# Performance work log

Measured on AMD Instinct MI355X. Metric: run time of the kernel, lower is better.

Reference implementation:

```python
import jax, jax.numpy as jnp
import numpy as np

NUM_HEADS = 4


def setup_inputs() -> dict:
    key = jax.random.key(0)
    ks = jax.random.split(key, 9)
    B, C, H, W = 8, 128, 48, 48
    s = 0.02
    return {
        "x": jax.random.normal(ks[0], (B, C, H, W), dtype=jnp.float32),
        "Wq": jax.random.normal(ks[1], (C, C), dtype=jnp.float32) * s,
        "bq": jax.random.normal(ks[2], (C,), dtype=jnp.float32) * s,
        "Wk": jax.random.normal(ks[3], (C, C), dtype=jnp.float32) * s,
        "bk": jax.random.normal(ks[4], (C,), dtype=jnp.float32) * s,
        "Wv": jax.random.normal(ks[5], (C, C), dtype=jnp.float32) * s,
        "bv": jax.random.normal(ks[6], (C,), dtype=jnp.float32) * s,
        "Wo": jax.random.normal(ks[7], (C, C), dtype=jnp.float32) * s,
        "bo": jax.random.normal(ks[8], (C,), dtype=jnp.float32) * s,
    }


def reference(x, Wq, bq, Wk, bk, Wv, bv, Wo, bo):
    B, C, H, W = x.shape
    nh = NUM_HEADS
    hd = C // nh  # head_size
    S = H * W
    # b c h w -> b (h w) c
    xf = x.reshape(B, C, S).transpose(0, 2, 1)
    # nn.Linear: y = x @ W.T + b ; split heads: b s (h d) -> b h s d
    q = (xf @ Wq.T + bq).reshape(B, S, nh, hd).transpose(0, 2, 1, 3)
    k = (xf @ Wk.T + bk).reshape(B, S, nh, hd).transpose(0, 2, 1, 3)
    v = (xf @ Wv.T + bv).reshape(B, S, nh, hd).transpose(0, 2, 1, 3)
    # scores: [B, nh, S, S]
    scores = jnp.einsum('bhqd,bhkd->bhqk', q, k) / jnp.sqrt(jnp.float32(hd)).astype(x.dtype)
    attn = jax.nn.softmax(scores, axis=-1)
    ctx = jnp.einsum('bhqk,bhkd->bhqd', attn, v)
    # merge heads: b h s d -> b s (h d)
    ctx = ctx.transpose(0, 2, 1, 3).reshape(B, S, C)
    out = ctx @ Wo.T + bo  # [B, S, C]
    # b (h w) c -> b c h w
    return out.transpose(0, 2, 1).reshape(B, C, H, W)
```

## Files before the change

kernel.cpp:

```cpp
#include <hip/hip_runtime.h>
#include <hip/hip_bf16.h>

typedef __attribute__((ext_vector_type(8))) short bf16x8;
typedef __attribute__((ext_vector_type(4))) float floatx4;

constexpr int NB  = 8;
constexpr int NC  = 128;
constexpr int NS  = 2304;
constexpr int NNH = 4;
constexpr float SCALE_LOG2E = 0.17677669529663687f * 1.4426950408889634f;

__device__ inline unsigned short f2bf(float f) {
    union { float f; unsigned u; } v; v.f = f;
    unsigned r = v.u + 0x7FFF + ((v.u >> 16) & 1);
    return (unsigned short)(r >> 16);
}

__device__ inline float fexp2(float x) {
#if __has_builtin(__builtin_amdgcn_exp2f)
    return __builtin_amdgcn_exp2f(x);
#else
    return exp2f(x);
#endif
}

__device__ inline __hip_bfloat162 pk(float a, float b) {
    return __float22bfloat162_rn(make_float2(a, b));
}

__global__ __launch_bounds__(256) void qkv_fused_kernel(
    const float* __restrict__ x,
    const float* __restrict__ Wq, const float* __restrict__ bq,
    const float* __restrict__ Wk, const float* __restrict__ bk,
    const float* __restrict__ Wv, const float* __restrict__ bv,
    unsigned short* __restrict__ Qb, unsigned short* __restrict__ Kb,
    unsigned short* __restrict__ Vb)
{
    const int s0 = blockIdx.x * 64;
    const int b  = blockIdx.y;
    const int t  = threadIdx.x;
    const int w = t >> 6, lane = t & 63;
    const int l15 = lane & 15, quad = lane >> 4;

    __shared__ __align__(16) char smem[34304];
    float* tileF = (float*)(smem + w * 4224);
    unsigned short* xs = (unsigned short*)(smem + 16896);

    #pragma unroll
    for (int sh = 0; sh < 2; ++sh) {
        #pragma unroll
        for (int it = 0; it < 16; ++it) {
            int c = it * 2 + (lane >> 5), sl = lane & 31;
            tileF[c * 33 + sl] =
                x[((size_t)b * NC + 32 * w + c) * NS + s0 + 32 * sh + sl];
        }
        #pragma unroll
        for (int it = 0; it < 16; ++it) {
            int s_l = it * 2 + (lane >> 5), c_l = lane & 31;
            xs[(32 * sh + s_l) * 136 + 32 * w + c_l] =
                f2bf(tileF[c_l * 33 + s_l]);
        }
    }
    __syncthreads();

    bf16x8 a[4][4];
    #pragma unroll
    for (int m = 0; m < 4; ++m)
        #pragma unroll
        for (int c = 0; c < 4; ++c)
            a[m][c] = *(const bf16x8*)&xs[(16 * m + l15) * 136 + 32 * c + 8 * quad];
    __syncthreads();

    const int h = w;
    const size_t bh = (size_t)(b * NNH + h);
    unsigned short* e = (unsigned short*)smem + (size_t)w * 2560;

    for (int p = 0; p < 3; ++p) {
        const float* Wsel = (p == 0) ? Wq : (p == 1) ? Wk : Wv;
        const float* bsel = (p == 0) ? bq : (p == 1) ? bk : bv;
        const float sc = (p == 0) ? SCALE_LOG2E : 1.0f;

        bf16x8 wf[2][4];
        #pragma unroll
        for (int n = 0; n < 2; ++n)
            #pragma unroll
            for (int c = 0; c < 4; ++c) {
                const float* wp = &Wsel[(size_t)(32 * w + 16 * n + l15) * NC + 32 * c + 8 * quad];
                float4 wa = *(const float4*)wp;
                float4 wb = *(const float4*)(wp + 4);
                union { bf16x8 v; __hip_bfloat162 h2[4]; } u;
                u.h2[0] = pk(wa.x, wa.y);
                u.h2[1] = pk(wa.z, wa.w);
                u.h2[2] = pk(wb.x, wb.y);
                u.h2[3] = pk(wb.z, wb.w);
                wf[n][c] = u.v;
            }

        floatx4 acc[4][2] = {};
        #pragma unroll
        for (int c = 0; c < 4; ++c)
            #pragma unroll
            for (int m = 0; m < 4; ++m)
                #pragma unroll
                for (int n = 0; n < 2; ++n)
                    acc[m][n] = __builtin_amdgcn_mfma_f32_16x16x32_bf16(
                        a[m][c], wf[n][c], acc[m][n], 0, 0, 0);

        const float bj0 = bsel[32 * w + l15];
        const float bj1 = bsel[32 * w + 16 + l15];

        #pragma unroll
        for (int m = 0; m < 4; ++m)
            #pragma unroll
            for (int r = 0; r < 4; ++r) {
                e[(16 * m + 4 * quad + r) * 40 + l15]      = f2bf((acc[m][0][r] + bj0) * sc);
                e[(16 * m + 4 * quad + r) * 40 + 16 + l15] = f2bf((acc[m][1][r] + bj1) * sc);
            }

        if (p < 2) {
            unsigned short* dst = (p == 0) ? Qb : Kb;
            const int s_l = lane >> 1, half = lane & 1;
            #pragma unroll
            for (int sh = 0; sh < 2; ++sh) {
                bf16x8 v0 = *(const bf16x8*)&e[(sh * 32 + s_l) * 40 + 16 * half];
                bf16x8 v1 = *(const bf16x8*)&e[(sh * 32 + s_l) * 40 + 16 * half + 8];
                unsigned short* g = &dst[(bh * NS + s0 + sh * 32 + s_l) * 32 + 16 * half];
                *(bf16x8*)g = v0;
                *(bf16x8*)(g + 8) = v1;
            }
        } else {
            const int d = lane >> 1, half = lane & 1;
            #pragma unroll
            for (int sh = 0; sh < 2; ++sh) {
                unsigned short tmp[16];
                #pragma unroll
                for (int i = 0; i < 16; ++i) {
                    int pos = 16 * half + i;
                    int kl = (((pos >> 2) & 1) << 4) | (((pos >> 3) & 3) << 2) | (pos & 3);
                    tmp[i] = e[(sh * 32 + kl) * 40 + d];
                }
                unsigned short* g = &Vb[(bh * 32 + d) * NS + s0 + sh * 32 + 16 * half];
                *(bf16x8*)g = *(bf16x8*)&tmp[0];
                *(bf16x8*)(g + 8) = *(bf16x8*)&tmp[8];
            }
        }
    }
}

__global__ __launch_bounds__(512) void attn_out_kernel(
    const unsigned short* __restrict__ Qb,
    const unsigned short* __restrict__ Kb,
    const unsigned short* __restrict__ Vb,
    const float* __restrict__ Wo, const float* __restrict__ bo,
    float* __restrict__ out)
{
    const int bid = blockIdx.x;
    const int qt = bid >> 3, b = bid & 7;
    const int t = threadIdx.x;
    const int w = t >> 6, lane = t & 63;
    const int l15 = lane & 15, quad = lane >> 4;
    const int h = w & 3, ks = w >> 2;

    const size_t bh = (size_t)(b * NNH + h);
    const unsigned short* Kp = Kb + bh * NS * 32;
    const unsigned short* Vp = Vb + bh * 32 * NS;
    const int q0g = qt * 64;

    __shared__ __align__(16) float Osum[4][64 * 36];
    __shared__ float Ls[4][64];
    __shared__ __align__(16) unsigned short ctxs[64 * 136];

    bf16x8 qf[4];
    #pragma unroll
    for (int g = 0; g < 4; ++g)
        qf[g] = *(const bf16x8*)&Qb[(bh * NS + q0g + g * 16 + l15) * 32 + quad * 8];

    float lsum[4] = {};
    floatx4 o[4][2] = {};

    const int kbase = ks * 18 * 64;
    bf16x8 kfc[4], vfc[4], kfn[4], vfn[4];
    #pragma unroll
    for (int n = 0; n < 4; ++n)
        kfc[n] = *(const bf16x8*)&Kp[(kbase + 16 * n + l15) * 32 + quad * 8];
    vfc[0] = *(const bf16x8*)&Vp[(0  + l15) * NS + kbase +  0 + 8 * quad];
    vfc[1] = *(const bf16x8*)&Vp[(0  + l15) * NS + kbase + 32 + 8 * quad];
    vfc[2] = *(const bf16x8*)&Vp[(16 + l15) * NS + kbase +  0 + 8 * quad];
    vfc[3] = *(const bf16x8*)&Vp[(16 + l15) * NS + kbase + 32 + 8 * quad];

    for (int it = 0; it < 18; ++it) {
        const int kn = kbase + ((it < 17) ? (it + 1) * 64 : 0);
        #pragma unroll
        for (int n = 0; n < 4; ++n)
            kfn[n] = *(const bf16x8*)&Kp[(kn + 16 * n + l15) * 32 + quad * 8];
        vfn[0] = *(const bf16x8*)&Vp[(0  + l15) * NS + kn +  0 + 8 * quad];
        vfn[1] = *(const bf16x8*)&Vp[(0  + l15) * NS + kn + 32 + 8 * quad];
        vfn[2] = *(const bf16x8*)&Vp[(16 + l15) * NS + kn +  0 + 8 * quad];
        vfn[3] = *(const bf16x8*)&Vp[(16 + l15) * NS + kn + 32 + 8 * quad];

        #pragma unroll
        for (int g = 0; g < 4; ++g) {
            floatx4 s[4];
            #pragma unroll
            for (int n = 0; n < 4; ++n) {
                floatx4 z = {0.f, 0.f, 0.f, 0.f};
                s[n] = __builtin_amdgcn_mfma_f32_16x16x32_bf16(kfc[n], qf[g], z, 0, 0, 0);
            }
            float p[4][4];
            #pragma unroll
            for (int n = 0; n < 4; ++n)
                #pragma unroll
                for (int r = 0; r < 4; ++r) {
                    p[n][r] = fexp2(s[n][r]);
                    lsum[g] += p[n][r];
                }
            union { bf16x8 v; __hip_bfloat162 h2[4]; } pf0, pf1;
            pf0.h2[0] = pk(p[0][0], p[0][1]);
            pf0.h2[1] = pk(p[0][2], p[0][3]);
            pf0.h2[2] = pk(p[1][0], p[1][1]);
            pf0.h2[3] = pk(p[1][2], p[1][3]);
            pf1.h2[0] = pk(p[2][0], p[2][1]);
            pf1.h2[1] = pk(p[2][2], p[2][3]);
            pf1.h2[2] = pk(p[3][0], p[3][1]);
            pf1.h2[3] = pk(p[3][2], p[3][3]);

            o[g][0] = __builtin_amdgcn_mfma_f32_16x16x32_bf16(vfc[0], pf0.v, o[g][0], 0, 0, 0);
            o[g][0] = __builtin_amdgcn_mfma_f32_16x16x32_bf16(vfc[1], pf1.v, o[g][0], 0, 0, 0);
            o[g][1] = __builtin_amdgcn_mfma_f32_16x16x32_bf16(vfc[2], pf0.v, o[g][1], 0, 0, 0);
            o[g][1] = __builtin_amdgcn_mfma_f32_16x16x32_bf16(vfc[3], pf1.v, o[g][1], 0, 0, 0);
        }

        #pragma unroll
        for (int n = 0; n < 4; ++n) { kfc[n] = kfn[n]; vfc[n] = vfn[n]; }
    }

    #pragma unroll
    for (int g = 0; g < 4; ++g) {
        lsum[g] += __shfl_xor(lsum[g], 16);
        lsum[g] += __shfl_xor(lsum[g], 32);
    }

    if (ks == 0) {
        #pragma unroll
        for (int g = 0; g < 4; ++g)
            #pragma unroll
            for (int m = 0; m < 2; ++m)
                *(floatx4*)&Osum[h][(g * 16 + l15) * 36 + m * 16 + 4 * quad] = o[g][m];
        if (quad == 0)
            #pragma unroll
            for (int g = 0; g < 4; ++g)
                Ls[h][g * 16 + l15] = lsum[g];
    }
    __syncthreads();
    if (ks == 1) {
        #pragma unroll
        for (int g = 0; g < 4; ++g) {
            const float inv = 1.f / (Ls[h][g * 16 + l15] + lsum[g]);
            #pragma unroll
            for (int m = 0; m < 2; ++m) {
                floatx4 part = *(const floatx4*)&Osum[h][(g * 16 + l15) * 36 + m * 16 + 4 * quad];
                floatx4 tot = part + o[g][m];
                unsigned short* cx = &ctxs[(g * 16 + l15) * 136 + h * 32 + m * 16 + 4 * quad];
                *(__hip_bfloat162*)&cx[0] = pk(tot[0] * inv, tot[1] * inv);
                *(__hip_bfloat162*)&cx[2] = pk(tot[2] * inv, tot[3] * inv);
            }
        }
    }
    __syncthreads();

    const int j0 = w * 16;
    bf16x8 wo[4];
    #pragma unroll
    for (int c = 0; c < 4; ++c) {
        const float* wp = &Wo[(size_t)(j0 + l15) * NC + 32 * c + 8 * quad];
        float4 wa = *(const float4*)wp;
        float4 wb = *(const float4*)(wp + 4);
        union { bf16x8 v; __hip_bfloat162 h2[4]; } u;
        u.h2[0] = pk(wa.x, wa.y);
        u.h2[1] = pk(wa.z, wa.w);
        u.h2[2] = pk(wb.x, wb.y);
        u.h2[3] = pk(wb.z, wb.w);
        wo[c] = u.v;
    }

    floatx4 oacc[4] = {};
    #pragma unroll
    for (int m = 0; m < 4; ++m)
        #pragma unroll
        for (int c = 0; c < 4; ++c) {
            bf16x8 cb = *(const bf16x8*)&ctxs[(16 * m + l15) * 136 + 32 * c + 8 * quad];
            oacc[m] = __builtin_amdgcn_mfma_f32_16x16x32_bf16(wo[c], cb, oacc[m], 0, 0, 0);
        }

    #pragma unroll
    for (int r = 0; r < 4; ++r) {
        const float bj = bo[j0 + 4 * quad + r];
        #pragma unroll
        for (int m = 0; m < 4; ++m)
            out[((size_t)b * NC + j0 + 4 * quad + r) * NS + q0g + 16 * m + l15] =
                oacc[m][r] + bj;
    }
}

extern "C" void kernel_launch(void* const* d_in, const int* in_sizes, int n_in,
                              void* d_out, int out_size, void* d_ws, size_t ws_size,
                              hipStream_t stream) {
    (void)in_sizes; (void)n_in; (void)out_size; (void)ws_size;
    const float* x  = (const float*)d_in[0];
    const float* Wq = (const float*)d_in[1];
    const float* bq = (const float*)d_in[2];
    const float* Wk = (const float*)d_in[3];
    const float* bk = (const float*)d_in[4];
    const float* Wv = (const float*)d_in[5];
    const float* bv = (const float*)d_in[6];
    const float* Wo = (const float*)d_in[7];
    const float* bo = (const float*)d_in[8];
    float* out = (float*)d_out;

    const size_t NTOK = (size_t)NB * NS * NC;
    unsigned short* Qb = (unsigned short*)d_ws;
    unsigned short* Kb = Qb + NTOK;
    unsigned short* Vb = Kb + NTOK;

    qkv_fused_kernel<<<dim3(36, NB), 256, 0, stream>>>(
        x, Wq, bq, Wk, bk, Wv, bv, Qb, Kb, Vb);
    attn_out_kernel<<<dim3(288), 512, 0, stream>>>(
        Qb, Kb, Vb, Wo, bo, out);
}
```

Baseline: 151.2 us.

## Split attention from output projection and raise parallelism across heads and key splits

```diff
diff --git a/kernel.cpp b/kernel.cpp
--- a/kernel.cpp
+++ b/kernel.cpp
@@ -36,36 +36,31 @@
     unsigned short* __restrict__ Qb, unsigned short* __restrict__ Kb,
     unsigned short* __restrict__ Vb)
 {
-    const int s0 = blockIdx.x * 64;
+    const int s0 = blockIdx.x * 32;
     const int b  = blockIdx.y;
     const int t  = threadIdx.x;
     const int w = t >> 6, lane = t & 63;
     const int l15 = lane & 15, quad = lane >> 4;
 
-    __shared__ __align__(16) char smem[34304];
+    __shared__ __align__(16) char smem[25600];
     float* tileF = (float*)(smem + w * 4224);
     unsigned short* xs = (unsigned short*)(smem + 16896);
 
     #pragma unroll
-    for (int sh = 0; sh < 2; ++sh) {
-        #pragma unroll
-        for (int it = 0; it < 16; ++it) {
-            int c = it * 2 + (lane >> 5), sl = lane & 31;
-            tileF[c * 33 + sl] =
-                x[((size_t)b * NC + 32 * w + c) * NS + s0 + 32 * sh + sl];
-        }
-        #pragma unroll
-        for (int it = 0; it < 16; ++it) {
-            int s_l = it * 2 + (lane >> 5), c_l = lane & 31;
-            xs[(32 * sh + s_l) * 136 + 32 * w + c_l] =
-                f2bf(tileF[c_l * 33 + s_l]);
-        }
+    for (int it = 0; it < 16; ++it) {
+        int c = it * 2 + (lane >> 5), sl = lane & 31;
+        tileF[c * 33 + sl] = x[((size_t)b * NC + 32 * w + c) * NS + s0 + sl];
+    }
+    #pragma unroll
+    for (int it = 0; it < 16; ++it) {
+        int s_l = it * 2 + (lane >> 5), c_l = lane & 31;
+        xs[s_l * 136 + 32 * w + c_l] = f2bf(tileF[c_l * 33 + s_l]);
     }
     __syncthreads();
 
-    bf16x8 a[4][4];
-    #pragma unroll
-    for (int m = 0; m < 4; ++m)
+    bf16x8 a[2][4];
+    #pragma unroll
+    for (int m = 0; m < 2; ++m)
         #pragma unroll
         for (int c = 0; c < 4; ++c)
             a[m][c] = *(const bf16x8*)&xs[(16 * m + l15) * 136 + 32 * c + 8 * quad];
@@ -73,7 +68,7 @@
 
     const int h = w;
     const size_t bh = (size_t)(b * NNH + h);
-    unsigned short* e = (unsigned short*)smem + (size_t)w * 2560;
+    unsigned short* e = (unsigned short*)smem + (size_t)w * 1280;
 
     for (int p = 0; p < 3; ++p) {
         const float* Wsel = (p == 0) ? Wq : (p == 1) ? Wk : Wv;
@@ -96,11 +91,11 @@
                 wf[n][c] = u.v;
             }
 
-        floatx4 acc[4][2] = {};
+        floatx4 acc[2][2] = {};
         #pragma unroll
         for (int c = 0; c < 4; ++c)
             #pragma unroll
-            for (int m = 0; m < 4; ++m)
+            for (int m = 0; m < 2; ++m)
                 #pragma unroll
                 for (int n = 0; n < 2; ++n)
                     acc[m][n] = __builtin_amdgcn_mfma_f32_16x16x32_bf16(
@@ -110,7 +105,7 @@
         const float bj1 = bsel[32 * w + 16 + l15];
 
         #pragma unroll
-        for (int m = 0; m < 4; ++m)
+        for (int m = 0; m < 2; ++m)
             #pragma unroll
             for (int r = 0; r < 4; ++r) {
                 e[(16 * m + 4 * quad + r) * 40 + l15]      = f2bf((acc[m][0][r] + bj0) * sc);
@@ -120,55 +115,48 @@
         if (p < 2) {
             unsigned short* dst = (p == 0) ? Qb : Kb;
             const int s_l = lane >> 1, half = lane & 1;
-            #pragma unroll
-            for (int sh = 0; sh < 2; ++sh) {
-                bf16x8 v0 = *(const bf16x8*)&e[(sh * 32 + s_l) * 40 + 16 * half];
-                bf16x8 v1 = *(const bf16x8*)&e[(sh * 32 + s_l) * 40 + 16 * half + 8];
-                unsigned short* g = &dst[(bh * NS + s0 + sh * 32 + s_l) * 32 + 16 * half];
-                *(bf16x8*)g = v0;
-                *(bf16x8*)(g + 8) = v1;
-            }
+            bf16x8 v0 = *(const bf16x8*)&e[s_l * 40 + 16 * half];
+            bf16x8 v1 = *(const bf16x8*)&e[s_l * 40 + 16 * half + 8];
+            unsigned short* g = &dst[(bh * NS + s0 + s_l) * 32 + 16 * half];
+            *(bf16x8*)g = v0;
+            *(bf16x8*)(g + 8) = v1;
         } else {
             const int d = lane >> 1, half = lane & 1;
-            #pragma unroll
-            for (int sh = 0; sh < 2; ++sh) {
-                unsigned short tmp[16];
-                #pragma unroll
-                for (int i = 0; i < 16; ++i) {
-                    int pos = 16 * half + i;
-                    int kl = (((pos >> 2) & 1) << 4) | (((pos >> 3) & 3) << 2) | (pos & 3);
-                    tmp[i] = e[(sh * 32 + kl) * 40 + d];
-                }
-                unsigned short* g = &Vb[(bh * 32 + d) * NS + s0 + sh * 32 + 16 * half];
-                *(bf16x8*)g = *(bf16x8*)&tmp[0];
-                *(bf16x8*)(g + 8) = *(bf16x8*)&tmp[8];
-            }
+            unsigned short tmp[16];
+            #pragma unroll
+            for (int i = 0; i < 16; ++i) {
+                int pos = 16 * half + i;
+                int kl = (((pos >> 2) & 1) << 4) | (((pos >> 3) & 3) << 2) | (pos & 3);
+                tmp[i] = e[kl * 40 + d];
+            }
+            unsigned short* g = &Vb[(bh * 32 + d) * NS + s0 + 16 * half];
+            *(bf16x8*)g = *(bf16x8*)&tmp[0];
+            *(bf16x8*)(g + 8) = *(bf16x8*)&tmp[8];
         }
     }
 }
 
-__global__ __launch_bounds__(512) void attn_out_kernel(
+__global__ __launch_bounds__(256) void attn_kernel(
     const unsigned short* __restrict__ Qb,
     const unsigned short* __restrict__ Kb,
     const unsigned short* __restrict__ Vb,
-    const float* __restrict__ Wo, const float* __restrict__ bo,
-    float* __restrict__ out)
+    unsigned short* __restrict__ ctxb)
 {
     const int bid = blockIdx.x;
-    const int qt = bid >> 3, b = bid & 7;
+    const int b = bid & 7;
+    const int rest = bid >> 3;
+    const int h = rest & 3, qt = rest >> 2;
     const int t = threadIdx.x;
-    const int w = t >> 6, lane = t & 63;
+    const int ks = t >> 6, lane = t & 63;
     const int l15 = lane & 15, quad = lane >> 4;
-    const int h = w & 3, ks = w >> 2;
 
     const size_t bh = (size_t)(b * NNH + h);
     const unsigned short* Kp = Kb + bh * NS * 32;
     const unsigned short* Vp = Vb + bh * 32 * NS;
     const int q0g = qt * 64;
 
-    __shared__ __align__(16) float Osum[4][64 * 36];
-    __shared__ float Ls[4][64];
-    __shared__ __align__(16) unsigned short ctxs[64 * 136];
+    __shared__ __align__(16) float Opart[3][64 * 36];
+    __shared__ float Lp[3][64];
 
     bf16x8 qf[4];
     #pragma unroll
@@ -178,7 +166,7 @@
     float lsum[4] = {};
     floatx4 o[4][2] = {};
 
-    const int kbase = ks * 18 * 64;
+    const int kbase = ks * 9 * 64;
     bf16x8 kfc[4], vfc[4], kfn[4], vfn[4];
     #pragma unroll
     for (int n = 0; n < 4; ++n)
@@ -188,8 +176,8 @@
     vfc[2] = *(const bf16x8*)&Vp[(16 + l15) * NS + kbase +  0 + 8 * quad];
     vfc[3] = *(const bf16x8*)&Vp[(16 + l15) * NS + kbase + 32 + 8 * quad];
 
-    for (int it = 0; it < 18; ++it) {
-        const int kn = kbase + ((it < 17) ? (it + 1) * 64 : 0);
+    for (int it = 0; it < 9; ++it) {
+        const int kn = kbase + ((it < 8) ? (it + 1) * 64 : 0);
         #pragma unroll
         for (int n = 0; n < 4; ++n)
             kfn[n] = *(const bf16x8*)&Kp[(kn + 16 * n + l15) * 32 + quad * 8];
@@ -210,10 +198,14 @@
             #pragma unroll
             for (int n = 0; n < 4; ++n)
                 #pragma unroll
-                for (int r = 0; r < 4; ++r) {
+                for (int r = 0; r < 4; ++r)
                     p[n][r] = fexp2(s[n][r]);
-                    lsum[g] += p[n][r];
-                }
+            float t0 = (p[0][0] + p[0][1]) + (p[0][2] + p[0][3]);
+            float t1 = (p[1][0] + p[1][1]) + (p[1][2] + p[1][3]);
+            float t2 = (p[2][0] + p[2][1]) + (p[2][2] + p[2][3]);
+            float t3 = (p[3][0] + p[3][1]) + (p[3][2] + p[3][3]);
+            lsum[g] += (t0 + t1) + (t2 + t3);
+
             union { bf16x8 v; __hip_bfloat162 h2[4]; } pf0, pf1;
             pf0.h2[0] = pk(p[0][0], p[0][1]);
             pf0.h2[1] = pk(p[0][2], p[0][3]);
@@ -240,35 +232,51 @@
         lsum[g] += __shfl_xor(lsum[g], 32);
     }
 
+    if (ks > 0) {
+        #pragma unroll
+        for (int g = 0; g < 4; ++g)
+            #pragma unroll
+            for (int m = 0; m < 2; ++m)
+                *(floatx4*)&Opart[ks - 1][(g * 16 + l15) * 36 + m * 16 + 4 * quad] = o[g][m];
+        if (quad == 0)
+            #pragma unroll
+            for (int g = 0; g < 4; ++g)
+                Lp[ks - 1][g * 16 + l15] = lsum[g];
+    }
+    __syncthreads();
     if (ks == 0) {
         #pragma unroll
-        for (int g = 0; g < 4; ++g)
-            #pragma unroll
-            for (int m = 0; m < 2; ++m)
-                *(floatx4*)&Osum[h][(g * 16 + l15) * 36 + m * 16 + 4 * quad] = o[g][m];
-        if (quad == 0)
-            #pragma unroll
-            for (int g = 0; g < 4; ++g)
-                Ls[h][g * 16 + l15] = lsum[g];
-    }
-    __syncthreads();
-    if (ks == 1) {
-        #pragma unroll
         for (int g = 0; g < 4; ++g) {
-            const float inv = 1.f / (Ls[h][g * 16 + l15] + lsum[g]);
+            const int q = g * 16 + l15;
+            const float inv =
+                1.f / (((lsum[g] + Lp[0][q]) + (Lp[1][q] + Lp[2][q])));
+            unsigned short* cp = &ctxb[((size_t)b * NS + q0g + q) * NC + h * 32];
             #pragma unroll
             for (int m = 0; m < 2; ++m) {
-                floatx4 part = *(const floatx4*)&Osum[h][(g * 16 + l15) * 36 + m * 16 + 4 * quad];
-                floatx4 tot = part + o[g][m];
-                unsigned short* cx = &ctxs[(g * 16 + l15) * 136 + h * 32 + m * 16 + 4 * quad];
-                *(__hip_bfloat162*)&cx[0] = pk(tot[0] * inv, tot[1] * inv);
-                *(__hip_bfloat162*)&cx[2] = pk(tot[2] * inv, tot[3] * inv);
+                floatx4 tot = o[g][m];
+                #pragma unroll
+                for (int i = 0; i < 3; ++i)
+                    tot += *(const floatx4*)&Opart[i][q * 36 + m * 16 + 4 * quad];
+                *(__hip_bfloat162*)&cp[m * 16 + 4 * quad]     = pk(tot[0] * inv, tot[1] * inv);
+                *(__hip_bfloat162*)&cp[m * 16 + 4 * quad + 2] = pk(tot[2] * inv, tot[3] * inv);
             }
         }
     }
-    __syncthreads();
-
-    const int j0 = w * 16;
+}
+
+__global__ __launch_bounds__(256) void out_proj_kernel(
+    const unsigned short* __restrict__ ctxb,
+    const float* __restrict__ Wo, const float* __restrict__ bo,
+    float* __restrict__ out)
+{
+    const int b = blockIdx.z;
+    const int t = threadIdx.x;
+    const int w = t >> 6, lane = t & 63;
+    const int l15 = lane & 15, quad = lane >> 4;
+
+    const int j0 = blockIdx.y * 64 + w * 16;
+    const int s0 = blockIdx.x * 64;
+
     bf16x8 wo[4];
     #pragma unroll
     for (int c = 0; c < 4; ++c) {
@@ -288,7 +296,7 @@
     for (int m = 0; m < 4; ++m)
         #pragma unroll
         for (int c = 0; c < 4; ++c) {
-            bf16x8 cb = *(const bf16x8*)&ctxs[(16 * m + l15) * 136 + 32 * c + 8 * quad];
+            bf16x8 cb = *(const bf16x8*)&ctxb[((size_t)b * NS + s0 + 16 * m + l15) * NC + 32 * c + 8 * quad];
             oacc[m] = __builtin_amdgcn_mfma_f32_16x16x32_bf16(wo[c], cb, oacc[m], 0, 0, 0);
         }
 
@@ -297,7 +305,7 @@
         const float bj = bo[j0 + 4 * quad + r];
         #pragma unroll
         for (int m = 0; m < 4; ++m)
-            out[((size_t)b * NC + j0 + 4 * quad + r) * NS + q0g + 16 * m + l15] =
+            out[((size_t)b * NC + j0 + 4 * quad + r) * NS + s0 + 16 * m + l15] =
                 oacc[m][r] + bj;
     }
 }
@@ -318,12 +326,13 @@
     float* out = (float*)d_out;
 
     const size_t NTOK = (size_t)NB * NS * NC;
-    unsigned short* Qb = (unsigned short*)d_ws;
-    unsigned short* Kb = Qb + NTOK;
-    unsigned short* Vb = Kb + NTOK;
-
-    qkv_fused_kernel<<<dim3(36, NB), 256, 0, stream>>>(
+    unsigned short* Qb   = (unsigned short*)d_ws;
+    unsigned short* Kb   = Qb + NTOK;
+    unsigned short* Vb   = Kb + NTOK;
+    unsigned short* ctxb = Vb + NTOK;
+
+    qkv_fused_kernel<<<dim3(72, NB), 256, 0, stream>>>(
         x, Wq, bq, Wk, bk, Wv, bv, Qb, Kb, Vb);
-    attn_out_kernel<<<dim3(288), 512, 0, stream>>>(
-        Qb, Kb, Vb, Wo, bo, out);
-}
+    attn_kernel<<<dim3(1152), 256, 0, stream>>>(Qb, Kb, Vb, ctxb);
+    out_proj_kernel<<<dim3(36, 2, NB), 256, 0, stream>>>(ctxb, Wo, bo, out);
+}
```

Measured after the change: 150.2 us. Within noise of the previous version (-0.6%).
